# Kernel optimization log

Hardware: AMD Instinct MI355X
Metric: run time of the kernel (lower is better)

Reference implementation:

```python
import jax, jax.numpy as jnp
import numpy as np

B, L, H = 2, 2048, 2048
NH, D = 16, 128          # num_heads, head_dim
MLP = 4 * H              # mlp_hidden_dim = int(hidden_size * mlp_ratio)


def setup_inputs() -> dict:
    key = jax.random.key(0)
    ks = jax.random.split(key, 8)
    x = jax.random.normal(ks[0], (B, L, H), jnp.float32)
    vec = jax.random.normal(ks[1], (B, H), jnp.float32)
    pe = jax.random.normal(ks[2], (B, 1, L, D // 2, 2, 2), jnp.float32)
    # Modulation(dim, is_double=False): Linear(H, 3H)
    mod_w = 0.02 * jax.random.normal(ks[3], (3 * H, H), jnp.float32)
    mod_b = jnp.zeros((3 * H,), jnp.float32)
    # linear1: Linear(H, 3H + MLP)
    lin1_w = 0.02 * jax.random.normal(ks[4], (3 * H + MLP, H), jnp.float32)
    lin1_b = jnp.zeros((3 * H + MLP,), jnp.float32)
    # linear2: Linear(H + MLP, H)
    lin2_w = 0.02 * jax.random.normal(ks[5], (H, H + MLP), jnp.float32)
    lin2_b = jnp.zeros((H,), jnp.float32)
    # QKNorm: RMSNorm scales over head_dim
    q_scale = jnp.ones((D,), jnp.float32)
    k_scale = jnp.ones((D,), jnp.float32)
    return dict(x=x, vec=vec, pe=pe, mod_w=mod_w, mod_b=mod_b,
                lin1_w=lin1_w, lin1_b=lin1_b, lin2_w=lin2_w, lin2_b=lin2_b,
                q_scale=q_scale, k_scale=k_scale)


def _layernorm(x, eps=1e-6):
    mu = jnp.mean(x, axis=-1, keepdims=True)
    var = jnp.mean((x - mu) ** 2, axis=-1, keepdims=True)
    return (x - mu) * jax.lax.rsqrt(var + eps)


def _rmsnorm(x, scale, eps=1e-6):
    return x * jax.lax.rsqrt(jnp.mean(x * x, axis=-1, keepdims=True) + eps) * scale


def _apply_rope(t, pe):
    # t: [B, NH, L, D]; pe: [B, 1, L, D//2, 2, 2]
    t_ = t.reshape(*t.shape[:-1], D // 2, 1, 2)
    out = pe[..., 0] * t_[..., 0] + pe[..., 1] * t_[..., 1]  # [B, NH, L, D//2, 2]
    return out.reshape(*t.shape)


def reference(x, vec, pe, mod_w, mod_b, lin1_w, lin1_b, lin2_w, lin2_b, q_scale, k_scale):
    # Modulation: silu -> linear -> (shift, scale, gate), each [B, 1, H]
    mod = jax.nn.silu(vec) @ mod_w.T + mod_b
    shift, scale, gate = jnp.split(mod[:, None, :], 3, axis=-1)

    x_mod = (1.0 + scale) * _layernorm(x) + shift

    h = x_mod @ lin1_w.T + lin1_b            # [B, L, 3H + MLP]
    qkv, mlp = h[..., :3 * H], h[..., 3 * H:]

    # 'B L (K H D) -> K B H L D'
    qkv = qkv.reshape(B, L, 3, NH, D).transpose(2, 0, 3, 1, 4)
    q, k, v = qkv[0], qkv[1], qkv[2]

    q = _rmsnorm(q, q_scale)
    k = _rmsnorm(k, k_scale)

    q = _apply_rope(q, pe)
    k = _apply_rope(k, pe)

    # SDPA with default scale 1/sqrt(D)
    logits = jnp.einsum('bhqd,bhkd->bhqk', q, k) / jnp.sqrt(jnp.float32(D))
    probs = jax.nn.softmax(logits, axis=-1)
    attn = jnp.einsum('bhqk,bhkd->bhqd', probs, v)          # [B, NH, L, D]
    attn = attn.transpose(0, 2, 1, 3).reshape(B, L, H)      # 'B H L D -> B L (H D)'

    mlp_act = jax.nn.gelu(mlp, approximate=True)
    out = jnp.concatenate([attn, mlp_act], axis=-1) @ lin2_w.T + lin2_b
    return x + gate * out
```

## Files before the change

### kernel.cpp

```cpp
#include <hip/hip_runtime.h>

#define LSEQ 2048
#define HDIM 2048
#define NHEAD 16
#define DHEAD 128
#define N1 14336
#define NC 10240

typedef unsigned short u16;
typedef __attribute__((ext_vector_type(8))) short short8;
typedef __attribute__((ext_vector_type(4))) float f32x4;

#define ASYNC16(g, l) __builtin_amdgcn_global_load_lds( \
    (__attribute__((address_space(1))) void*)(g),        \
    (__attribute__((address_space(3))) void*)(l), 16, 0, 0)

__device__ __forceinline__ u16 f2bf(float f) {
  unsigned u = __builtin_bit_cast(unsigned, f);
  u += 0x7fffu + ((u >> 16) & 1u);
  return (u16)(u >> 16);
}
__device__ __forceinline__ u16 f2bf_trunc(float f) {
  return (u16)(__builtin_bit_cast(unsigned, f) >> 16);
}
__device__ __forceinline__ float bf2f(u16 v) {
  unsigned u = ((unsigned)v) << 16;
  return __builtin_bit_cast(float, u);
}
__device__ __forceinline__ float silu_f(float x) { return x / (1.f + __expf(-x)); }
__device__ __forceinline__ float gelu_f(float x) {
  float u = 0.7978845608028654f * (x + 0.044715f * x * x * x);
  float e = __expf(2.f * u);
  float th = 1.f - 2.f / (e + 1.f);
  return 0.5f * x * (1.f + th);
}

__global__ __launch_bounds__(256) void k_mod(const float* __restrict__ vec,
                                             const float* __restrict__ mod_w,
                                             const float* __restrict__ mod_b,
                                             float* __restrict__ modv) {
  int j = blockIdx.x, t = threadIdx.x;
  const float4* wr = (const float4*)(mod_w + (size_t)j * HDIM);
  const float4* vv = (const float4*)vec;
  float s0 = 0.f, s1 = 0.f;
#pragma unroll
  for (int i = 0; i < 2; i++) {
    int idx = t + i * 256;
    float4 w = wr[idx];
    float4 a = vv[idx];
    float4 c = vv[idx + 512];
    s0 += w.x*silu_f(a.x) + w.y*silu_f(a.y) + w.z*silu_f(a.z) + w.w*silu_f(a.w);
    s1 += w.x*silu_f(c.x) + w.y*silu_f(c.y) + w.z*silu_f(c.z) + w.w*silu_f(c.w);
  }
  int lane = t & 63, wid = t >> 6;
#pragma unroll
  for (int o = 32; o; o >>= 1) { s0 += __shfl_down(s0, o, 64); s1 += __shfl_down(s1, o, 64); }
  __shared__ float red[8];
  if (!lane) { red[wid] = s0; red[4 + wid] = s1; }
  __syncthreads();
  if (!t) {
    float b_ = mod_b[j];
    modv[j] = red[0]+red[1]+red[2]+red[3] + b_;
    modv[3*HDIM + j] = red[4]+red[5]+red[6]+red[7] + b_;
  }
}

__global__ __launch_bounds__(256) void k_ln(const float* __restrict__ x,
                                            const float* __restrict__ modv,
                                            u16* __restrict__ xmod) {
  int row = blockIdx.x, t = threadIdx.x;
  int b = row >> 11;
  const float4* xr = (const float4*)(x + (size_t)row * HDIM);
  float4 v0 = xr[t], v1 = xr[t + 256];
  float sum = v0.x+v0.y+v0.z+v0.w + v1.x+v1.y+v1.z+v1.w;
  float sq  = v0.x*v0.x+v0.y*v0.y+v0.z*v0.z+v0.w*v0.w
            + v1.x*v1.x+v1.y*v1.y+v1.z*v1.z+v1.w*v1.w;
  int lane = t & 63, wid = t >> 6;
#pragma unroll
  for (int o = 32; o; o >>= 1) { sum += __shfl_down(sum, o, 64); sq += __shfl_down(sq, o, 64); }
  __shared__ float red[8];
  if (!lane) { red[wid] = sum; red[4+wid] = sq; }
  __syncthreads();
  sum = red[0]+red[1]+red[2]+red[3];
  sq  = red[4]+red[5]+red[6]+red[7];
  float mu = sum * (1.f/HDIM);
  float rstd = rsqrtf(sq * (1.f/HDIM) - mu*mu + 1e-6f);
  const float* mb = modv + b * (3*HDIM);
  u16* orow = xmod + (size_t)row * HDIM;
  float vv[8] = {v0.x,v0.y,v0.z,v0.w,v1.x,v1.y,v1.z,v1.w};
#pragma unroll
  for (int half = 0; half < 2; half++) {
    int h0 = (t + half*256) * 4;
    ushort4 o4;
    float e0 = (1.f + mb[HDIM + h0+0]) * ((vv[half*4+0]-mu)*rstd) + mb[h0+0];
    float e1 = (1.f + mb[HDIM + h0+1]) * ((vv[half*4+1]-mu)*rstd) + mb[h0+1];
    float e2 = (1.f + mb[HDIM + h0+2]) * ((vv[half*4+2]-mu)*rstd) + mb[h0+2];
    float e3 = (1.f + mb[HDIM + h0+3]) * ((vv[half*4+3]-mu)*rstd) + mb[h0+3];
    o4.x = f2bf(e0); o4.y = f2bf(e1); o4.z = f2bf(e2); o4.w = f2bf(e3);
    *(ushort4*)(orow + h0) = o4;
  }
}

__global__ __launch_bounds__(256) void k_cvt(const float4* __restrict__ src,
                                             ushort4* __restrict__ dst, int n4) {
  int i = blockIdx.x * 256 + threadIdx.x;
  int stride = gridDim.x * 256;
  for (; i < n4; i += stride) {
    float4 v = src[i];
    ushort4 o;
    o.x = f2bf(v.x); o.y = f2bf(v.y); o.z = f2bf(v.z); o.w = f2bf(v.w);
    dst[i] = o;
  }
}

#define FENCE asm volatile("" ::: "memory")
#define BARRIER { FENCE; __builtin_amdgcn_s_barrier(); FENCE; }
#define WAITVM(n) asm volatile("s_waitcnt vmcnt(" #n ")" ::: "memory")

#define ABUF(bufv) (S + (bufv)*16384)
#define BBUF(bufv) (S + 32768 + (bufv)*16384)

#define STG_A(bufv, rbase, kk) do { \
    int r_ = (rbase) + wave * 8; \
    ASYNC16(Ab + (size_t)(r_ + lr) * K + (kk) + sg * 8, ABUF(bufv) + r_ * 64); \
  } while (0)
#define STG_B(bufv, rbase, kk) do { \
    int r_ = (rbase) + (wave >> 2) * 64 + (wave & 3) * 8; \
    ASYNC16(Bb + (size_t)(r_ + lr) * K + (kk) + sg * 8, BBUF(bufv) + r_ * 64); \
  } while (0)
#define STG_U0(bufv, kk) { STG_A(bufv, 0, kk);   STG_A(bufv, 128, kk); }
#define STG_U1(bufv, kk) { STG_A(bufv, 64, kk);  STG_A(bufv, 192, kk); }
#define STG_U2(bufv, kk) { STG_B(bufv, 0, kk);   STG_B(bufv, 128, kk); }
#define STG_U3(bufv, kk) { STG_B(bufv, 32, kk);  STG_B(bufv, 160, kk); }

#define LDS_A(qmv, bufv) do { \
    const u16* p_ = ABUF(bufv); \
    _Pragma("unroll") for (int mt = 0; mt < 4; mt++) { \
      int row_ = wm*128 + (qmv)*64 + mt*16 + fm; \
      _Pragma("unroll") for (int ks = 0; ks < 2; ks++) \
        a[mt][ks] = *(const short8*)(p_ + row_*64 + (((ks*4 + fq) ^ (fm & 7)) * 8)); \
    } } while (0)
#define LDS_Bv(dst, qnv, bufv) do { \
    const u16* p_ = BBUF(bufv); \
    _Pragma("unroll") for (int nt = 0; nt < 2; nt++) { \
      int row_ = wn*64 + (qnv)*32 + nt*16 + fm; \
      _Pragma("unroll") for (int ks = 0; ks < 2; ks++) \
        dst[nt][ks] = *(const short8*)(p_ + row_*64 + (((ks*4 + fq) ^ (fm & 7)) * 8)); \
    } } while (0)

#define MMQ(qmv, qnv, bsel) do { \
    __builtin_amdgcn_s_setprio(1); \
    _Pragma("unroll") for (int mt = 0; mt < 4; mt++) \
    _Pragma("unroll") for (int nt = 0; nt < 2; nt++) \
    _Pragma("unroll") for (int ks = 0; ks < 2; ks++) \
      acc[(qmv)*4 + mt][(qnv)*2 + nt] = __builtin_amdgcn_mfma_f32_16x16x32_bf16( \
          a[mt][ks], bsel[nt][ks], acc[(qmv)*4 + mt][(qnv)*2 + nt], 0, 0, 0); \
    __builtin_amdgcn_s_setprio(0); } while (0)

#define PHASE_Q00(bufv, STAGE, VMN) { LDS_A(0, bufv); LDS_Bv(b0, 0, bufv); STAGE; BARRIER; \
                                      MMQ(0, 0, b0); WAITVM(VMN); BARRIER; }
#define PHASE_Q01(bufv, STAGE, VMN) { LDS_Bv(b1, 1, bufv); STAGE; BARRIER; \
                                      MMQ(0, 1, b1); WAITVM(VMN); BARRIER; }
#define PHASE_Q11(bufv, STAGE, VMN) { LDS_A(1, bufv); STAGE; BARRIER; \
                                      MMQ(1, 1, b1); WAITVM(VMN); BARRIER; }
#define PHASE_Q10(bufv, STAGE, VMN) { STAGE; BARRIER; \
                                      MMQ(1, 0, b0); WAITVM(VMN); BARRIER; }

__global__ __launch_bounds__(512, 2) void k_gemm1(const u16* __restrict__ A,
                                                  const u16* __restrict__ Bw,
                                                  const float* __restrict__ bias,
                                                  u16* __restrict__ qkv,
                                                  u16* __restrict__ cat) {
  const int K = HDIM;
  const int NT = K / 64;
  int orig = blockIdx.x;
  int bid = (orig & 7) * 112 + (orig >> 3);
  int bm = bid & 15, bn = bid >> 4;
  int t = threadIdx.x, wave = t >> 6, lane = t & 63;
  int wm = wave >> 2, wn = wave & 3;
  int fm = lane & 15, fq = lane >> 4;
  int lr = lane >> 3, lg = lane & 7;
  int sg = lg ^ lr;

  __shared__ u16 S[65536];

  const u16* Ab = A + (size_t)bm * 256 * K;
  const u16* Bb = Bw + (size_t)bn * 256 * K;

  const f32x4 fzero = {0.f, 0.f, 0.f, 0.f};
  f32x4 acc[8][4];
#pragma unroll
  for (int i = 0; i < 8; i++)
#pragma unroll
    for (int j2 = 0; j2 < 4; j2++) acc[i][j2] = fzero;
  short8 a[4][2], b0[2][2], b1[2][2];

  STG_U0(0, 0); STG_U2(0, 0); STG_U3(0, 0); STG_U1(0, 0);
  WAITVM(4); BARRIER;

  const int NIT = NT / 2;
  for (int it2 = 0; it2 < NIT - 1; ++it2) {
    int kB = it2 * 128 + 64;
    int kC = it2 * 128 + 128;
    PHASE_Q00(0, STG_U0(1, kB), 4);
    PHASE_Q01(0, STG_U2(1, kB), 4);
    PHASE_Q11(0, STG_U3(1, kB), 4);
    PHASE_Q10(0, STG_U1(1, kB), 4);
    PHASE_Q00(1, STG_U0(0, kC), 4);
    PHASE_Q01(1, STG_U2(0, kC), 4);
    PHASE_Q11(1, STG_U3(0, kC), 4);
    PHASE_Q10(1, STG_U1(0, kC), 4);
  }
  {
    int kB = (NT - 1) * 64;
    PHASE_Q00(0, STG_U0(1, kB), 4);
    PHASE_Q01(0, STG_U2(1, kB), 4);
    PHASE_Q11(0, STG_U3(1, kB), 4);
    PHASE_Q10(0, STG_U1(1, kB), 4);
    PHASE_Q00(1, ((void)0), 2);
    PHASE_Q01(1, ((void)0), 0);
    PHASE_Q11(1, ((void)0), 0);
    PHASE_Q10(1, ((void)0), 0);
  }

  bool ismlp = (bn >= 24);
  const int EP = 264;
  u16* Sep = S;
#pragma unroll
  for (int half = 0; half < 2; half++) {
    BARRIER;
    if (wm == half) {
#pragma unroll
      for (int j = 0; j < 4; j++) {
        int col_l = wn*64 + j*16 + fm;
        float bv = bias[bn*256 + col_l];
#pragma unroll
        for (int i = 0; i < 8; i++) {
#pragma unroll
          for (int rr = 0; rr < 4; rr++) {
            float v = acc[i][j][rr] + bv;
            if (ismlp) v = gelu_f(v);
            Sep[(i*16 + fq*4 + rr)*EP + col_l] = f2bf(v);
          }
        }
      }
    }
    BARRIER;
    int cg = (t & 31) * 8;
    int r0 = t >> 5;
#pragma unroll
    for (int p = 0; p < 8; p++) {
      int r_l = p*16 + r0;
      short8 v = *(const short8*)&Sep[r_l*EP + cg];
      int row_g = bm*256 + half*128 + r_l;
      if (!ismlp)
        *(short8*)(qkv + (size_t)row_g*(3*HDIM) + bn*256 + cg) = v;
      else
        *(short8*)(cat + (size_t)row_g*NC + HDIM + (bn-24)*256 + cg) = v;
    }
  }
}

__global__ __launch_bounds__(256, 2) void k_gemm2(const u16* __restrict__ A,
                                                  const u16* __restrict__ Bw,
                                                  const float* __restrict__ bias,
                                                  const float* __restrict__ xres,
                                                  const float* __restrict__ modv,
                                                  float* __restrict__ out) {
  const int K = NC;
  int bid = blockIdx.x;
  int bm = bid & 31, bn = bid >> 5;
  int t = threadIdx.x, wave = t >> 6, lane = t & 63;
  int wm = wave >> 1, wn = wave & 1;
  __shared__ u16 As[2*128*32];
  __shared__ u16 Bs[2*128*32];
  const f32x4 fzero = {0.f, 0.f, 0.f, 0.f};
  f32x4 acc[4][4];
#pragma unroll
  for (int i = 0; i < 4; i++)
#pragma unroll
    for (int j2 = 0; j2 < 4; j2++) acc[i][j2] = fzero;
  const u16* Ab = A + (size_t)bm * 128 * K;
  const u16* Bb = Bw + (size_t)bn * 128 * K;
  int r4 = lane >> 2, c4 = lane & 3;
  int fm = lane & 15, fk = (lane >> 4) * 8;
  for (int k0 = 0; k0 < K; k0 += 64) {
#pragma unroll
    for (int i = 0; i < 2; i++) {
      int row = wave*32 + i*16;
      const u16* ar = Ab + (size_t)(row + r4)*K + k0 + c4*8;
      const u16* br = Bb + (size_t)(row + r4)*K + k0 + c4*8;
      ASYNC16(ar,      &As[row*32]);
      ASYNC16(ar + 32, &As[4096 + row*32]);
      ASYNC16(br,      &Bs[row*32]);
      ASYNC16(br + 32, &Bs[4096 + row*32]);
    }
    __syncthreads();
#pragma unroll
    for (int p = 0; p < 2; p++) {
      const u16* Ap = &As[p*4096];
      const u16* Bp = &Bs[p*4096];
      short8 af[4], bfr[4];
#pragma unroll
      for (int mt = 0; mt < 4; mt++)
        af[mt] = *(const short8*)&Ap[(wm*64 + mt*16 + fm)*32 + fk];
#pragma unroll
      for (int nt = 0; nt < 4; nt++)
        bfr[nt] = *(const short8*)&Bp[(wn*64 + nt*16 + fm)*32 + fk];
#pragma unroll
      for (int mt = 0; mt < 4; mt++)
#pragma unroll
        for (int nt = 0; nt < 4; nt++)
          acc[mt][nt] = __builtin_amdgcn_mfma_f32_16x16x32_bf16(af[mt], bfr[nt], acc[mt][nt], 0, 0, 0);
    }
    __syncthreads();
  }
  int rbase = bm*128 + wm*64;
  int cbase = bn*128 + wn*64;
  int b = (bm*128) >> 11;
#pragma unroll
  for (int nt = 0; nt < 4; nt++) {
    int col = cbase + nt*16 + fm;
    float bv = bias[col];
    float g = modv[b*(3*HDIM) + 2*HDIM + col];
#pragma unroll
    for (int mt = 0; mt < 4; mt++) {
#pragma unroll
      for (int rr = 0; rr < 4; rr++) {
        int row = rbase + mt*16 + (lane>>4)*4 + rr;
        size_t idx = (size_t)row*HDIM + col;
        out[idx] = xres[idx] + g * (acc[mt][nt][rr] + bv);
      }
    }
  }
}

__global__ __launch_bounds__(256) void k_qk(const u16* __restrict__ qkv,
                                            const float* __restrict__ pe,
                                            const float* __restrict__ q_scale,
                                            const float* __restrict__ k_scale,
                                            u16* __restrict__ Q, u16* __restrict__ Ko) {
  int bid = blockIdx.x;
  int l = bid & (LSEQ-1);
  int b = bid >> 11;
  int t = threadIdx.x;
  int h = t >> 4;
  int dc = (t & 15) * 8;
  const u16* base = qkv + (size_t)bid * (3*HDIM);
  short8 q8 = *(const short8*)(base + h*DHEAD + dc);
  short8 k8 = *(const short8*)(base + HDIM + h*DHEAD + dc);
  float qf[8], kf[8];
  float sq = 0.f, sk = 0.f;
#pragma unroll
  for (int i = 0; i < 8; i++) {
    qf[i] = bf2f((u16)q8[i]); kf[i] = bf2f((u16)k8[i]);
    sq += qf[i]*qf[i]; sk += kf[i]*kf[i];
  }
#pragma unroll
  for (int m = 1; m < 16; m <<= 1) { sq += __shfl_xor(sq, m, 64); sk += __shfl_xor(sk, m, 64); }
  float rq = rsqrtf(sq * (1.f/DHEAD) + 1e-6f);
  float rk = rsqrtf(sk * (1.f/DHEAD) + 1e-6f);
  float4 qs0 = *(const float4*)(q_scale + dc), qs1 = *(const float4*)(q_scale + dc + 4);
  float4 ks0 = *(const float4*)(k_scale + dc), ks1 = *(const float4*)(k_scale + dc + 4);
  float qsc[8] = {qs0.x,qs0.y,qs0.z,qs0.w,qs1.x,qs1.y,qs1.z,qs1.w};
  float ksc[8] = {ks0.x,ks0.y,ks0.z,ks0.w,ks1.x,ks1.y,ks1.z,ks1.w};
  float qn[8], kn[8];
#pragma unroll
  for (int i = 0; i < 8; i++) { qn[i] = qf[i]*rq*qsc[i]; kn[i] = kf[i]*rk*ksc[i]; }
  const float4* pe4 = (const float4*)pe + ((size_t)bid*64 + (dc >> 1));
  short8 qo, ko;
#pragma unroll
  for (int pi = 0; pi < 4; pi++) {
    float4 pp = pe4[pi];
    float q0 = pp.x*qn[2*pi] + pp.y*qn[2*pi+1];
    float q1 = pp.z*qn[2*pi] + pp.w*qn[2*pi+1];
    float k0 = pp.x*kn[2*pi] + pp.y*kn[2*pi+1];
    float k1 = pp.z*kn[2*pi] + pp.w*kn[2*pi+1];
    qo[2*pi] = (short)f2bf(q0); qo[2*pi+1] = (short)f2bf(q1);
    ko[2*pi] = (short)f2bf(k0); ko[2*pi+1] = (short)f2bf(k1);
  }
  size_t oidx = (((size_t)(b*NHEAD + h))*LSEQ + l)*DHEAD + dc;
  *(short8*)(Q + oidx) = qo;
  *(short8*)(Ko + oidx) = ko;
}

__global__ __launch_bounds__(256) void k_vt(const u16* __restrict__ qkv, u16* __restrict__ Vt) {
  int bid = blockIdx.x;
  int lt = bid & 31, h = (bid >> 5) & 15, b = bid >> 9;
  __shared__ u16 tile[64][132];
  int t = threadIdx.x;
#pragma unroll
  for (int it = 0; it < 8; it++) {
    int idx = it*1024 + t*4;
    int li = idx >> 7, di = idx & 127;
    const u16* src = qkv + ((size_t)(b*LSEQ + lt*64 + li))*(3*HDIM) + 2*HDIM + h*DHEAD + di;
    ushort4 v = *(const ushort4*)src;
    *(ushort4*)&tile[li][di] = v;
  }
  __syncthreads();
  u16* dst = Vt + ((size_t)(b*NHEAD + h))*DHEAD*LSEQ + lt*64;
#pragma unroll
  for (int it = 0; it < 32; it++) {
    int idx = it*256 + t;
    int lo = idx & 63, dd = idx >> 6;
    dst[(size_t)dd*LSEQ + lo] = tile[lo][dd];
  }
}

#define SC2 0.12753329583f
__global__ __launch_bounds__(256, 2) void k_attn(const u16* __restrict__ Q,
                                                 const u16* __restrict__ Kc,
                                                 const u16* __restrict__ Vt,
                                                 u16* __restrict__ cat) {
  __shared__ u16 Ks[2*64*128];
  __shared__ u16 Vs[2*128*64];
  __shared__ u16 Ps[64*88];
  int bid = blockIdx.x;
  int bh = bid & 31, qt = bid >> 5;
  int h = bh & 15, b = bh >> 4;
  int t = threadIdx.x, wave = t >> 6, lane = t & 63;
  int fm = lane & 15, fq = lane >> 4;
  int r8 = lane >> 3, c8 = lane & 7;
  const u16* Qg = Q  + (((size_t)(b*NHEAD + h))*LSEQ + qt*64) * DHEAD;
  const u16* Kg = Kc + ((size_t)(b*NHEAD + h))*LSEQ * DHEAD;
  const u16* Vg = Vt + ((size_t)(b*NHEAD + h))*DHEAD*LSEQ;
  short8 aq[4];
#pragma unroll
  for (int ks = 0; ks < 4; ks++)
    aq[ks] = *(const short8*)(Qg + (size_t)(wave*16 + fm)*DHEAD + ks*32 + fq*8);
#pragma unroll
  for (int i = 0; i < 4; i++) {
    int row = wave*16 + i*4;
    ASYNC16(Kg + (size_t)(row + fq)*DHEAD + fm*8, &Ks[row*DHEAD]);
    int vrow = wave*32 + i*8;
    ASYNC16(Vg + (size_t)(vrow + r8)*LSEQ + c8*8, &Vs[vrow*64]);
  }
  const f32x4 fzero = {0.f, 0.f, 0.f, 0.f};
  f32x4 o[8];
#pragma unroll
  for (int i = 0; i < 8; i++) o[i] = fzero;
  float lsum[4] = {0.f, 0.f, 0.f, 0.f};
  for (int kt = 0; kt < 32; kt++) {
    int cur = kt & 1;
    __syncthreads();
    if (kt < 31) {
      int off = (cur ^ 1) * 8192;
      const u16* Kt_ = Kg + (size_t)(kt+1)*64*DHEAD;
      const u16* Vt_ = Vg + (kt+1)*64;
#pragma unroll
      for (int i = 0; i < 4; i++) {
        int row = wave*16 + i*4;
        ASYNC16(Kt_ + (size_t)(row + fq)*DHEAD + fm*8, &Ks[off + row*DHEAD]);
        int vrow = wave*32 + i*8;
        ASYNC16(Vt_ + (size_t)(vrow + r8)*LSEQ + c8*8, &Vs[off + vrow*64]);
      }
    }
    const u16* Kb = &Ks[cur*8192];
    const u16* Vb = &Vs[cur*8192];
    f32x4 s[4];
#pragma unroll
    for (int nt = 0; nt < 4; nt++) s[nt] = fzero;
#pragma unroll
    for (int ks = 0; ks < 4; ks++) {
#pragma unroll
      for (int nt = 0; nt < 4; nt++) {
        short8 bk = *(const short8*)&Kb[(nt*16 + fm)*DHEAD + ks*32 + fq*8];
        s[nt] = __builtin_amdgcn_mfma_f32_16x16x32_bf16(aq[ks], bk, s[nt], 0, 0, 0);
      }
    }
#pragma unroll
    for (int nt = 0; nt < 4; nt++)
#pragma unroll
      for (int r = 0; r < 4; r++) {
        float p = exp2f(s[nt][r] * SC2);
        s[nt][r] = p;
        lsum[r] += p;
      }
#pragma unroll
    for (int nt = 0; nt < 4; nt++)
#pragma unroll
      for (int r = 0; r < 4; r++)
        Ps[(wave*16 + fq*4 + r)*88 + nt*16 + fm] = f2bf_trunc(s[nt][r]);
    asm volatile("s_waitcnt lgkmcnt(0)" ::: "memory");
#pragma unroll
    for (int ks2 = 0; ks2 < 2; ks2++) {
      short8 ap = *(const short8*)&Ps[(wave*16 + fm)*88 + ks2*32 + fq*8];
#pragma unroll
      for (int nt = 0; nt < 8; nt++) {
        short8 bv = *(const short8*)&Vb[(nt*16 + fm)*64 + ks2*32 + fq*8];
        o[nt] = __builtin_amdgcn_mfma_f32_16x16x32_bf16(ap, bv, o[nt], 0, 0, 0);
      }
    }
  }
#pragma unroll
  for (int r = 0; r < 4; r++) {
#pragma unroll
    for (int o2 = 8; o2 >= 1; o2 >>= 1) lsum[r] += __shfl_xor(lsum[r], o2, 64);
  }
#pragma unroll
  for (int nt = 0; nt < 8; nt++) {
#pragma unroll
    for (int r = 0; r < 4; r++) {
      int l = qt*64 + wave*16 + fq*4 + r;
      int d = nt*16 + fm;
      float v = o[nt][r] / lsum[r];
      cat[((size_t)(b*LSEQ + l))*NC + h*DHEAD + d] = f2bf(v);
    }
  }
}

extern "C" void kernel_launch(void* const* d_in, const int* in_sizes, int n_in,
                              void* d_out, int out_size, void* d_ws, size_t ws_size,
                              hipStream_t stream) {
  const float* x       = (const float*)d_in[0];
  const float* vec     = (const float*)d_in[1];
  const float* pe      = (const float*)d_in[2];
  const float* mod_w   = (const float*)d_in[3];
  const float* mod_b   = (const float*)d_in[4];
  const float* lin1_w  = (const float*)d_in[5];
  const float* lin1_b  = (const float*)d_in[6];
  const float* lin2_w  = (const float*)d_in[7];
  const float* lin2_b  = (const float*)d_in[8];
  const float* q_scale = (const float*)d_in[9];
  const float* k_scale = (const float*)d_in[10];
  char* ws = (char*)d_ws;

  float* modv = (float*)(ws + 0);
  u16* xmod  = (u16*)(ws + 65536ULL);
  u16* qkv   = (u16*)(ws + 16842752ULL);
  u16* w2    = (u16*)(ws + 16842752ULL);
  u16* cat   = (u16*)(ws + 67174400ULL);
  u16* w1    = (u16*)(ws + 151060480ULL);
  u16* Qb    = (u16*)(ws + 151060480ULL);
  u16* Kb    = (u16*)(ws + 167837696ULL);
  u16* Vtb   = (u16*)(ws + 184614912ULL);

  k_mod<<<dim3(3*HDIM), dim3(256), 0, stream>>>(vec, mod_w, mod_b, modv);
  k_cvt<<<dim3(4096), dim3(256), 0, stream>>>((const float4*)lin1_w, (ushort4*)w1, (N1*HDIM)/4);
  k_ln<<<dim3(4096), dim3(256), 0, stream>>>(x, modv, xmod);
  k_gemm1<<<dim3(896), dim3(512), 0, stream>>>(xmod, w1, lin1_b, qkv, cat);
  k_qk<<<dim3(4096), dim3(256), 0, stream>>>(qkv, pe, q_scale, k_scale, Qb, Kb);
  k_vt<<<dim3(1024), dim3(256), 0, stream>>>(qkv, Vtb);
  k_cvt<<<dim3(4096), dim3(256), 0, stream>>>((const float4*)lin2_w, (ushort4*)w2, (HDIM*NC)/4);
  k_attn<<<dim3(1024), dim3(256), 0, stream>>>(Qb, Kb, Vtb, cat);
  k_gemm2<<<dim3(32*16), dim3(256), 0, stream>>>(cat, w2, lin2_b, x, modv, (float*)d_out);
}
```

Before: 1.034 ms.

## Restructure GEMM1 main loop with double-buffered A registers and deeper prefetch

Replaces the four-phase quadrant schedule in the first GEMM with a per-tile macro that loads both B fragments up front and keeps two A register sets. The next tile's A fragment is read from LDS during the current tile's MFMAs, and the global-to-LDS stages are issued earlier with different vmcnt waits. The goal is to hide LDS read latency and reduce stalls between MFMA groups. The cost is more registers under the 512-thread, 2-block launch bound and a more fragile wait and barrier ordering.

```diff
diff --git a/kernel.cpp b/kernel.cpp
--- a/kernel.cpp
+++ b/kernel.cpp
@@ -133,12 +133,12 @@
 #define STG_U2(bufv, kk) { STG_B(bufv, 0, kk);   STG_B(bufv, 128, kk); }
 #define STG_U3(bufv, kk) { STG_B(bufv, 32, kk);  STG_B(bufv, 160, kk); }
 
-#define LDS_A(qmv, bufv) do { \
+#define LDS_A(dst, qmv, bufv) do { \
     const u16* p_ = ABUF(bufv); \
     _Pragma("unroll") for (int mt = 0; mt < 4; mt++) { \
       int row_ = wm*128 + (qmv)*64 + mt*16 + fm; \
       _Pragma("unroll") for (int ks = 0; ks < 2; ks++) \
-        a[mt][ks] = *(const short8*)(p_ + row_*64 + (((ks*4 + fq) ^ (fm & 7)) * 8)); \
+        dst[mt][ks] = *(const short8*)(p_ + row_*64 + (((ks*4 + fq) ^ (fm & 7)) * 8)); \
     } } while (0)
 #define LDS_Bv(dst, qnv, bufv) do { \
     const u16* p_ = BBUF(bufv); \
@@ -148,23 +148,38 @@
         dst[nt][ks] = *(const short8*)(p_ + row_*64 + (((ks*4 + fq) ^ (fm & 7)) * 8)); \
     } } while (0)
 
-#define MMQ(qmv, qnv, bsel) do { \
+#define MMQ(qmv, qnv, Aa, Bv) do { \
     __builtin_amdgcn_s_setprio(1); \
     _Pragma("unroll") for (int mt = 0; mt < 4; mt++) \
     _Pragma("unroll") for (int nt = 0; nt < 2; nt++) \
     _Pragma("unroll") for (int ks = 0; ks < 2; ks++) \
       acc[(qmv)*4 + mt][(qnv)*2 + nt] = __builtin_amdgcn_mfma_f32_16x16x32_bf16( \
-          a[mt][ks], bsel[nt][ks], acc[(qmv)*4 + mt][(qnv)*2 + nt], 0, 0, 0); \
+          Aa[mt][ks], Bv[nt][ks], acc[(qmv)*4 + mt][(qnv)*2 + nt], 0, 0, 0); \
     __builtin_amdgcn_s_setprio(0); } while (0)
 
-#define PHASE_Q00(bufv, STAGE, VMN) { LDS_A(0, bufv); LDS_Bv(b0, 0, bufv); STAGE; BARRIER; \
-                                      MMQ(0, 0, b0); WAITVM(VMN); BARRIER; }
-#define PHASE_Q01(bufv, STAGE, VMN) { LDS_Bv(b1, 1, bufv); STAGE; BARRIER; \
-                                      MMQ(0, 1, b1); WAITVM(VMN); BARRIER; }
-#define PHASE_Q11(bufv, STAGE, VMN) { LDS_A(1, bufv); STAGE; BARRIER; \
-                                      MMQ(1, 1, b1); WAITVM(VMN); BARRIER; }
-#define PHASE_Q10(bufv, STAGE, VMN) { STAGE; BARRIER; \
-                                      MMQ(1, 0, b0); WAITVM(VMN); BARRIER; }
+#define GTILE(bufv, k1, k2, S01, RDA0, S2, S3, W1, W3) do { \
+     \
+    LDS_Bv(b0r, 0, bufv); \
+    LDS_Bv(b1r, 1, bufv); \
+    if (S01) { STG_U3((bufv)^1, k1); STG_U1((bufv)^1, k1); } \
+    BARRIER; \
+    MMQ(0, 0, areg0, b0r); \
+     \
+    LDS_A(areg1, 1, bufv); \
+    W1; \
+    BARRIER; \
+    MMQ(0, 1, areg0, b1r); \
+     \
+    if (RDA0) LDS_A(areg0, 0, (bufv)^1); \
+    if (S2) STG_U0(bufv, k2); \
+    BARRIER; \
+    MMQ(1, 1, areg1, b1r); \
+     \
+    if (S3) STG_U2(bufv, k2); \
+    W3; \
+    BARRIER; \
+    MMQ(1, 0, areg1, b0r); \
+  } while (0)
 
 __global__ __launch_bounds__(512, 2) void k_gemm1(const u16* __restrict__ A,
                                                   const u16* __restrict__ Bw,
@@ -172,7 +187,6 @@
                                                   u16* __restrict__ qkv,
                                                   u16* __restrict__ cat) {
   const int K = HDIM;
-  const int NT = K / 64;
   int orig = blockIdx.x;
   int bid = (orig & 7) * 112 + (orig >> 3);
   int bm = bid & 15, bn = bid >> 4;
@@ -193,35 +207,22 @@
   for (int i = 0; i < 8; i++)
 #pragma unroll
     for (int j2 = 0; j2 < 4; j2++) acc[i][j2] = fzero;
-  short8 a[4][2], b0[2][2], b1[2][2];
+  short8 areg0[4][2], areg1[4][2], b0r[2][2], b1r[2][2];
 
   STG_U0(0, 0); STG_U2(0, 0); STG_U3(0, 0); STG_U1(0, 0);
-  WAITVM(4); BARRIER;
-
-  const int NIT = NT / 2;
-  for (int it2 = 0; it2 < NIT - 1; ++it2) {
-    int kB = it2 * 128 + 64;
-    int kC = it2 * 128 + 128;
-    PHASE_Q00(0, STG_U0(1, kB), 4);
-    PHASE_Q01(0, STG_U2(1, kB), 4);
-    PHASE_Q11(0, STG_U3(1, kB), 4);
-    PHASE_Q10(0, STG_U1(1, kB), 4);
-    PHASE_Q00(1, STG_U0(0, kC), 4);
-    PHASE_Q01(1, STG_U2(0, kC), 4);
-    PHASE_Q11(1, STG_U3(0, kC), 4);
-    PHASE_Q10(1, STG_U1(0, kC), 4);
-  }
-  {
-    int kB = (NT - 1) * 64;
-    PHASE_Q00(0, STG_U0(1, kB), 4);
-    PHASE_Q01(0, STG_U2(1, kB), 4);
-    PHASE_Q11(0, STG_U3(1, kB), 4);
-    PHASE_Q10(0, STG_U1(1, kB), 4);
-    PHASE_Q00(1, ((void)0), 2);
-    PHASE_Q01(1, ((void)0), 0);
-    PHASE_Q11(1, ((void)0), 0);
-    PHASE_Q10(1, ((void)0), 0);
-  }
+  STG_U0(1, 64);
+  STG_U2(1, 64);
+  WAITVM(4);
+  BARRIER;
+  LDS_A(areg0, 0, 0);
+
+  for (int t2 = 0; t2 < 15; ++t2) {
+    int k0 = t2 * 128;
+    GTILE(0, k0+64,  k0+128, 1, 1, 1, 1, WAITVM(6), WAITVM(4));
+    GTILE(1, k0+128, k0+192, 1, 1, 1, 1, WAITVM(6), WAITVM(4));
+  }
+  GTILE(0, 31*64, 0, 1, 1, 0, 0, WAITVM(6), WAITVM(0));
+  GTILE(1, 0,     0, 0, 0, 0, 0, ((void)0), ((void)0));
 
   bool ismlp = (bn >= 24);
   const int EP = 264;
```

Measured after the change: 1.390 ms. +34.4%, slower.
